# Performance work log

Hardware: AMD Instinct MI355X
Metric: run time of the kernel (lower is better)

The kernel has to match this reference:

```python
import jax, jax.numpy as jnp
import numpy as np

N_NODES = 100000
N_EDGES = 1600000
STATE_DIM = 128
HID = 32


def _glorot(key, shape):
    fan_in, fan_out = shape
    lim = jnp.sqrt(6.0 / (fan_in + fan_out))
    return jax.random.uniform(key, shape, jnp.float32, -lim, lim)


def setup_inputs() -> dict:
    key = jax.random.key(0)
    ks = jax.random.split(key, 10)
    x = jax.random.normal(ks[0], (N_NODES, STATE_DIM), jnp.float32)
    edge_index = jax.random.randint(ks[1], (2, N_EDGES), 0, N_NODES, jnp.int32)
    params = {
        "W1": _glorot(ks[2], (STATE_DIM, HID)), "b1": jnp.zeros((HID,), jnp.float32),
        "Wh": _glorot(ks[3], (HID, HID)),        "bh": jnp.zeros((HID,), jnp.float32),
        "W2": _glorot(ks[4], (HID, 1)),          "b2": jnp.zeros((1,), jnp.float32),
        "Ws": _glorot(ks[5], (HID, 1)),          "bs": jnp.zeros((1,), jnp.float32),
    }
    return {"x": x, "edge_index": edge_index, **params}


def _gcn_norm(edge_index, n):
    # PyG GCNConv: add self-loops, symmetric normalization D^-1/2 (A+I) D^-1/2
    src, dst = edge_index[0], edge_index[1]
    ones = jnp.ones((src.shape[0],), jnp.float32)
    deg = jax.ops.segment_sum(ones, dst, num_segments=n) + 1.0  # +1 for self-loop
    dinv = jax.lax.rsqrt(deg)  # deg >= 1, always finite
    edge_norm = dinv[src] * dinv[dst]          # [E]
    self_norm = dinv * dinv                    # [N]
    return edge_norm, self_norm


def _gcn_conv(h, W, b, src, dst, edge_norm, self_norm, n):
    # transform first (PyG order), then normalized aggregation
    h = h @ W                                                   # [N, out]
    msg = h[src] * edge_norm[:, None]                           # [E, out] gather
    agg = jax.ops.segment_sum(msg, dst, num_segments=n)         # scatter-add
    return agg + h * self_norm[:, None] + b


def reference(x, edge_index, W1, b1, Wh, bh, W2, b2, Ws, bs):
    n = x.shape[0]
    src, dst = edge_index[0], edge_index[1]
    edge_norm, self_norm = _gcn_norm(edge_index, n)
    h = _gcn_conv(x, W1, b1, src, dst, edge_norm, self_norm, n)
    h = _gcn_conv(h, Wh, bh, src, dst, edge_norm, self_norm, n)
    mu = jax.nn.relu(h)
    mu = _gcn_conv(mu, W2, b2, src, dst, edge_norm, self_norm, n)
    std = _gcn_conv(h, Ws, bs, src, dst, edge_norm, self_norm, n)
    return (mu, std)
```

## Files before the change

kernel.cpp:

```cpp
#include <hip/hip_runtime.h>

#define NN 100000
#define NE 1600000
#define SD 128
#define HD 32
#define NV4 25000
#define NSB 98

__global__ __launch_bounds__(256) void k_count(const int* __restrict__ dst,
                                               unsigned* __restrict__ cnt,
                                               unsigned* __restrict__ rank) {
    int e = blockIdx.x * 256 + threadIdx.x;
    int d = dst[e];
    rank[e] = atomicAdd(&cnt[d], 1u);
}

__global__ __launch_bounds__(256) void k_scanA(const uint4* __restrict__ cnt4,
                                               unsigned* __restrict__ bsum) {
    __shared__ unsigned ts[256];
    int tid = threadIdx.x;
    int f = blockIdx.x * 256 + tid;
    unsigned s = 0;
    if (f < NV4) { uint4 v = cnt4[f]; s = v.x + v.y + v.z + v.w; }
    ts[tid] = s; __syncthreads();
    for (int off = 128; off > 0; off >>= 1) {
        if (tid < off) ts[tid] += ts[tid + off];
        __syncthreads();
    }
    if (tid == 0) bsum[blockIdx.x] = ts[0];
}

__global__ __launch_bounds__(128) void k_scanB(unsigned* __restrict__ bsum,
                                               unsigned* __restrict__ rowptr) {
    __shared__ unsigned s[128];
    int tid = threadIdx.x;
    unsigned v = (tid < NSB) ? bsum[tid] : 0u;
    s[tid] = v; __syncthreads();
    for (int off = 1; off < 128; off <<= 1) {
        unsigned t = (tid >= off) ? s[tid - off] : 0u;
        __syncthreads();
        s[tid] += t;
        __syncthreads();
    }
    if (tid < NSB) bsum[tid] = s[tid] - v;
    if (tid == 0) rowptr[NN] = NE;
}

__global__ __launch_bounds__(256) void k_scanC(const uint4* __restrict__ cnt4,
                                               const unsigned* __restrict__ bsum,
                                               uint4* __restrict__ rowptr4,
                                               float4* __restrict__ dinv4) {
    __shared__ unsigned ts[256];
    int tid = threadIdx.x;
    int f = blockIdx.x * 256 + tid;
    uint4 v = {0, 0, 0, 0};
    if (f < NV4) v = cnt4[f];
    unsigned tsum = v.x + v.y + v.z + v.w;
    ts[tid] = tsum; __syncthreads();
    for (int off = 1; off < 256; off <<= 1) {
        unsigned t = (tid >= off) ? ts[tid - off] : 0u;
        __syncthreads();
        ts[tid] += t;
        __syncthreads();
    }
    unsigned ebase = ts[tid] - tsum + bsum[blockIdx.x];
    if (f < NV4) {
        uint4 r;
        r.x = ebase;
        r.y = r.x + v.x;
        r.z = r.y + v.y;
        r.w = r.z + v.z;
        rowptr4[f] = r;
        float4 dv;
        dv.x = rsqrtf((float)v.x + 1.0f);
        dv.y = rsqrtf((float)v.y + 1.0f);
        dv.z = rsqrtf((float)v.z + 1.0f);
        dv.w = rsqrtf((float)v.w + 1.0f);
        dinv4[f] = dv;
    }
}

__global__ __launch_bounds__(256) void k_fill(const int* __restrict__ src,
                                              const int* __restrict__ dst,
                                              const unsigned* __restrict__ rank,
                                              const unsigned* __restrict__ rowptr,
                                              unsigned* __restrict__ edat) {
    int e = blockIdx.x * 256 + threadIdx.x;
    int d = dst[e];
    edat[rowptr[d] + rank[e]] = (unsigned)src[e];
}

__global__ __launch_bounds__(256) void k_mm128(const float* __restrict__ X,
                                               const float* __restrict__ W,
                                               const float* __restrict__ dinv,
                                               float* __restrict__ out) {
    __shared__ float Wls[SD * HD];
    __shared__ float xT[32][260];
    int tid = threadIdx.x;
    {
        const float4* W4 = (const float4*)W;
        float4* Wl4 = (float4*)Wls;
        for (int i = tid; i < SD * HD / 4; i += 256) Wl4[i] = W4[i];
    }
    int nb = blockIdx.x * 256;
    int g = tid & 7;
    int q = tid >> 3;
    float acc[8][4] = {};
    for (int kc = 0; kc < SD; kc += 32) {
        __syncthreads();
        for (int i = tid; i < 256 * 8; i += 256) {
            int n = i >> 3, k4 = i & 7;
            int node = nb + n;
            float4 v = (node < NN) ? *(const float4*)&X[(size_t)node * SD + kc + k4 * 4]
                                   : make_float4(0.f, 0.f, 0.f, 0.f);
            xT[k4 * 4 + 0][n] = v.x;
            xT[k4 * 4 + 1][n] = v.y;
            xT[k4 * 4 + 2][n] = v.z;
            xT[k4 * 4 + 3][n] = v.w;
        }
        __syncthreads();
#pragma unroll
        for (int kk = 0; kk < 32; ++kk) {
            const float4 xa = *(const float4*)&xT[kk][q * 8];
            const float4 xb = *(const float4*)&xT[kk][q * 8 + 4];
            const float4 wv = *(const float4*)&Wls[(kc + kk) * HD + g * 4];
            acc[0][0] = fmaf(xa.x, wv.x, acc[0][0]);
            acc[0][1] = fmaf(xa.x, wv.y, acc[0][1]);
            acc[0][2] = fmaf(xa.x, wv.z, acc[0][2]);
            acc[0][3] = fmaf(xa.x, wv.w, acc[0][3]);
            acc[1][0] = fmaf(xa.y, wv.x, acc[1][0]);
            acc[1][1] = fmaf(xa.y, wv.y, acc[1][1]);
            acc[1][2] = fmaf(xa.y, wv.z, acc[1][2]);
            acc[1][3] = fmaf(xa.y, wv.w, acc[1][3]);
            acc[2][0] = fmaf(xa.z, wv.x, acc[2][0]);
            acc[2][1] = fmaf(xa.z, wv.y, acc[2][1]);
            acc[2][2] = fmaf(xa.z, wv.z, acc[2][2]);
            acc[2][3] = fmaf(xa.z, wv.w, acc[2][3]);
            acc[3][0] = fmaf(xa.w, wv.x, acc[3][0]);
            acc[3][1] = fmaf(xa.w, wv.y, acc[3][1]);
            acc[3][2] = fmaf(xa.w, wv.z, acc[3][2]);
            acc[3][3] = fmaf(xa.w, wv.w, acc[3][3]);
            acc[4][0] = fmaf(xb.x, wv.x, acc[4][0]);
            acc[4][1] = fmaf(xb.x, wv.y, acc[4][1]);
            acc[4][2] = fmaf(xb.x, wv.z, acc[4][2]);
            acc[4][3] = fmaf(xb.x, wv.w, acc[4][3]);
            acc[5][0] = fmaf(xb.y, wv.x, acc[5][0]);
            acc[5][1] = fmaf(xb.y, wv.y, acc[5][1]);
            acc[5][2] = fmaf(xb.y, wv.z, acc[5][2]);
            acc[5][3] = fmaf(xb.y, wv.w, acc[5][3]);
            acc[6][0] = fmaf(xb.z, wv.x, acc[6][0]);
            acc[6][1] = fmaf(xb.z, wv.y, acc[6][1]);
            acc[6][2] = fmaf(xb.z, wv.z, acc[6][2]);
            acc[6][3] = fmaf(xb.z, wv.w, acc[6][3]);
            acc[7][0] = fmaf(xb.w, wv.x, acc[7][0]);
            acc[7][1] = fmaf(xb.w, wv.y, acc[7][1]);
            acc[7][2] = fmaf(xb.w, wv.z, acc[7][2]);
            acc[7][3] = fmaf(xb.w, wv.w, acc[7][3]);
        }
    }
#pragma unroll
    for (int r = 0; r < 8; ++r) {
        int node = nb + q * 8 + r;
        if (node < NN) {
            float dv = dinv[node];
            float4 o = {acc[r][0] * dv, acc[r][1] * dv, acc[r][2] * dv, acc[r][3] * dv};
            *(float4*)&out[(size_t)node * HD + g * 4] = o;
        }
    }
}

template <int MODE>
__global__ __launch_bounds__(256) void k_gather(const unsigned* __restrict__ edat,
                                                const unsigned* __restrict__ rowptr,
                                                const float* __restrict__ dinv,
                                                const float* __restrict__ hw,
                                                const float* __restrict__ bias,
                                                const float* __restrict__ Wa,
                                                const float* __restrict__ Wb,
                                                float* __restrict__ outw) {
    int gid = blockIdx.x * 256 + threadIdx.x;
    int n = gid >> 5, j = gid & 31;
    unsigned s0 = rowptr[n], s1 = rowptr[n + 1];
    float acc = 0.f;
    unsigned i = s0;
    for (; i + 4 <= s1; i += 4) {
        unsigned e0 = edat[i], e1 = edat[i + 1], e2 = edat[i + 2], e3 = edat[i + 3];
        float v0 = hw[(size_t)e0 * HD + j];
        float v1 = hw[(size_t)e1 * HD + j];
        float v2 = hw[(size_t)e2 * HD + j];
        float v3 = hw[(size_t)e3 * HD + j];
        acc += (v0 + v1) + (v2 + v3);
    }
    for (; i < s1; ++i) acc += hw[(size_t)edat[i] * HD + j];
    float dv = dinv[n];
    float v = dv * (acc + hw[(size_t)n * HD + j]) + bias[j];
    if (MODE == 1) {
        float h2 = 0.f;
#pragma unroll
        for (int jj = 0; jj < 32; ++jj)
            h2 = fmaf(__shfl(v, jj, 32), Wa[jj * HD + j], h2);
        outw[(size_t)n * HD + j] = h2 * dv;
    } else {
        float a = fmaxf(v, 0.f) * Wa[j];
        float b = v * Wb[j];
#pragma unroll
        for (int off = 16; off > 0; off >>= 1) {
            a += __shfl_xor(a, off, 32);
            b += __shfl_xor(b, off, 32);
        }
        if (j == 0) ((float2*)outw)[n] = make_float2(a * dv, b * dv);
    }
}

__global__ __launch_bounds__(256) void k_gscal(const unsigned* __restrict__ edat,
                                               const unsigned* __restrict__ rowptr,
                                               const float* __restrict__ dinv,
                                               const float2* __restrict__ head_w,
                                               const float* __restrict__ b2,
                                               const float* __restrict__ bs,
                                               float* __restrict__ out) {
    int gid = blockIdx.x * 256 + threadIdx.x;
    int n = gid >> 5, l = gid & 31;
    unsigned s0 = rowptr[n], s1 = rowptr[n + 1];
    float a = 0.f, b = 0.f;
    for (unsigned i = s0 + l; i < s1; i += 32) {
        float2 w = head_w[edat[i]];
        a += w.x; b += w.y;
    }
#pragma unroll
    for (int off = 16; off > 0; off >>= 1) {
        a += __shfl_xor(a, off, 32);
        b += __shfl_xor(b, off, 32);
    }
    if (l == 0) {
        float dv = dinv[n];
        float2 self = head_w[n];
        out[n]      = dv * (a + self.x) + b2[0];
        out[NN + n] = dv * (b + self.y) + bs[0];
    }
}

extern "C" void kernel_launch(void* const* d_in, const int* in_sizes, int n_in,
                              void* d_out, int out_size, void* d_ws, size_t ws_size,
                              hipStream_t stream) {
    const float* x   = (const float*)d_in[0];
    const int*   ei  = (const int*)d_in[1];
    const int*   src = ei;
    const int*   dst = ei + NE;
    const float* W1  = (const float*)d_in[2];
    const float* b1  = (const float*)d_in[3];
    const float* Wh  = (const float*)d_in[4];
    const float* bh  = (const float*)d_in[5];
    const float* W2  = (const float*)d_in[6];
    const float* b2  = (const float*)d_in[7];
    const float* Wsp = (const float*)d_in[8];
    const float* bs  = (const float*)d_in[9];
    float* out = (float*)d_out;

    unsigned* w      = (unsigned*)d_ws;
    unsigned* edat   = w;
    float*    hw1    = (float*)(w + 1600000);
    unsigned* rank   = w + 4800000;
    float*    hw2    = (float*)(w + 4800000);
    unsigned* rowptr = w + 8000000;
    unsigned* cnt    = rowptr + 100004;
    float*    dinv   = (float*)(cnt + 100000);
    float*    headw  = dinv + 100000;
    unsigned* bsum   = (unsigned*)(headw + 200000);

    hipMemsetAsync(cnt, 0, NN * sizeof(unsigned), stream);
    k_count<<<NE / 256, 256, 0, stream>>>(dst, cnt, rank);
    k_scanA<<<NSB, 256, 0, stream>>>((const uint4*)cnt, bsum);
    k_scanB<<<1, 128, 0, stream>>>(bsum, rowptr);
    k_scanC<<<NSB, 256, 0, stream>>>((const uint4*)cnt, bsum, (uint4*)rowptr, (float4*)dinv);
    k_fill<<<NE / 256, 256, 0, stream>>>(src, dst, rank, rowptr, edat);

    k_mm128<<<(NN + 255) / 256, 256, 0, stream>>>(x, W1, dinv, hw1);
    k_gather<1><<<NN * HD / 256, 256, 0, stream>>>(edat, rowptr, dinv, hw1, b1, Wh, nullptr, hw2);
    k_gather<2><<<NN * HD / 256, 256, 0, stream>>>(edat, rowptr, dinv, hw2, bh, W2, Wsp, headw);
    k_gscal<<<NN * HD / 256, 256, 0, stream>>>(edat, rowptr, dinv, (const float2*)headw, b2, bs, out);
}
```

Baseline: 333.3 us.

## Build CSR with two-level bucketed counting sort instead of global atomics

Replaces the per-edge global-atomic count, three-kernel scan and scattered fill with a bucketed counting sort. Edges are first binned by dst>>8 into 391 buckets using LDS histograms and block-level offsets. Each bucket is then sorted locally in shared memory to produce rowptr, dinv and the sorted source list. This removes global atomic contention and random global scatters. It relies on each bucket holding at most 6144 edges (MAXBE) and on packing the local dst index into the high bits of the src value.

```diff
diff --git a/kernel.cpp b/kernel.cpp
--- a/kernel.cpp
+++ b/kernel.cpp
@@ -4,90 +4,101 @@
 #define NE 1600000
 #define SD 128
 #define HD 32
-#define NV4 25000
-#define NSB 98
-
-__global__ __launch_bounds__(256) void k_count(const int* __restrict__ dst,
-                                               unsigned* __restrict__ cnt,
-                                               unsigned* __restrict__ rank) {
-    int e = blockIdx.x * 256 + threadIdx.x;
-    int d = dst[e];
-    rank[e] = atomicAdd(&cnt[d], 1u);
-}
-
-__global__ __launch_bounds__(256) void k_scanA(const uint4* __restrict__ cnt4,
-                                               unsigned* __restrict__ bsum) {
-    __shared__ unsigned ts[256];
+#define NBK 391
+#define EPB 4000
+#define NBLK 400
+#define MAXBE 6144
+
+__global__ __launch_bounds__(256) void k_p1(const int* __restrict__ dst,
+                                            unsigned* __restrict__ bktcnt,
+                                            unsigned* __restrict__ blockbase) {
+    __shared__ unsigned h[NBK];
+    int blk = blockIdx.x, tid = threadIdx.x;
+    for (int i = tid; i < NBK; i += 256) h[i] = 0;
+    __syncthreads();
+    int e0 = blk * EPB;
+    for (int i = tid; i < EPB; i += 256)
+        atomicAdd(&h[(unsigned)dst[e0 + i] >> 8], 1u);
+    __syncthreads();
+    for (int i = tid; i < NBK; i += 256)
+        blockbase[blk * NBK + i] = atomicAdd(&bktcnt[i], h[i]);
+}
+
+__global__ __launch_bounds__(512) void k_p2(const unsigned* __restrict__ bktcnt,
+                                            unsigned* __restrict__ bktbase,
+                                            unsigned* __restrict__ rowptr) {
+    __shared__ unsigned sc[512];
     int tid = threadIdx.x;
-    int f = blockIdx.x * 256 + tid;
-    unsigned s = 0;
-    if (f < NV4) { uint4 v = cnt4[f]; s = v.x + v.y + v.z + v.w; }
-    ts[tid] = s; __syncthreads();
-    for (int off = 128; off > 0; off >>= 1) {
-        if (tid < off) ts[tid] += ts[tid + off];
-        __syncthreads();
-    }
-    if (tid == 0) bsum[blockIdx.x] = ts[0];
-}
-
-__global__ __launch_bounds__(128) void k_scanB(unsigned* __restrict__ bsum,
-                                               unsigned* __restrict__ rowptr) {
-    __shared__ unsigned s[128];
-    int tid = threadIdx.x;
-    unsigned v = (tid < NSB) ? bsum[tid] : 0u;
-    s[tid] = v; __syncthreads();
-    for (int off = 1; off < 128; off <<= 1) {
-        unsigned t = (tid >= off) ? s[tid - off] : 0u;
-        __syncthreads();
-        s[tid] += t;
-        __syncthreads();
-    }
-    if (tid < NSB) bsum[tid] = s[tid] - v;
+    unsigned c = (tid < NBK) ? bktcnt[tid] : 0u;
+    sc[tid] = c;
+    __syncthreads();
+    for (int off = 1; off < 512; off <<= 1) {
+        unsigned t = (tid >= off) ? sc[tid - off] : 0u;
+        __syncthreads();
+        sc[tid] += t;
+        __syncthreads();
+    }
+    if (tid <= NBK) bktbase[tid] = sc[tid] - c;
     if (tid == 0) rowptr[NN] = NE;
 }
 
-__global__ __launch_bounds__(256) void k_scanC(const uint4* __restrict__ cnt4,
-                                               const unsigned* __restrict__ bsum,
-                                               uint4* __restrict__ rowptr4,
-                                               float4* __restrict__ dinv4) {
-    __shared__ unsigned ts[256];
-    int tid = threadIdx.x;
-    int f = blockIdx.x * 256 + tid;
-    uint4 v = {0, 0, 0, 0};
-    if (f < NV4) v = cnt4[f];
-    unsigned tsum = v.x + v.y + v.z + v.w;
-    ts[tid] = tsum; __syncthreads();
+__global__ __launch_bounds__(256) void k_p3(const int* __restrict__ src,
+                                            const int* __restrict__ dst,
+                                            const unsigned* __restrict__ bktbase,
+                                            const unsigned* __restrict__ blockbase,
+                                            unsigned* __restrict__ ebuf) {
+    __shared__ unsigned cur[NBK];
+    int blk = blockIdx.x, tid = threadIdx.x;
+    for (int i = tid; i < NBK; i += 256)
+        cur[i] = bktbase[i] + blockbase[blk * NBK + i];
+    __syncthreads();
+    int e0 = blk * EPB;
+    for (int i = tid; i < EPB; i += 256) {
+        int d = dst[e0 + i];
+        unsigned s = (unsigned)src[e0 + i];
+        unsigned b = (unsigned)d >> 8;
+        unsigned pos = atomicAdd(&cur[b], 1u);
+        ebuf[pos] = ((unsigned)(d & 255) << 20) | s;
+    }
+}
+
+__global__ __launch_bounds__(256) void k_p4(unsigned* __restrict__ ebuf,
+                                            const unsigned* __restrict__ bktbase,
+                                            unsigned* __restrict__ rowptr,
+                                            float* __restrict__ dinv) {
+    __shared__ unsigned eL[MAXBE];
+    __shared__ unsigned hist[256];
+    __shared__ unsigned sc[256];
+    int b = blockIdx.x, tid = threadIdx.x;
+    unsigned base = bktbase[b], nE = bktbase[b + 1] - base;
+    int n0 = b << 8;
+    int nodes = min(256, NN - n0);
+    for (unsigned i = tid; i < nE; i += 256) eL[i] = ebuf[base + i];
+    hist[tid] = 0;
+    __syncthreads();
+    for (unsigned i = tid; i < nE; i += 256) atomicAdd(&hist[eL[i] >> 20], 1u);
+    __syncthreads();
+    unsigned c = hist[tid];
+    sc[tid] = c;
+    __syncthreads();
     for (int off = 1; off < 256; off <<= 1) {
-        unsigned t = (tid >= off) ? ts[tid - off] : 0u;
-        __syncthreads();
-        ts[tid] += t;
-        __syncthreads();
-    }
-    unsigned ebase = ts[tid] - tsum + bsum[blockIdx.x];
-    if (f < NV4) {
-        uint4 r;
-        r.x = ebase;
-        r.y = r.x + v.x;
-        r.z = r.y + v.y;
-        r.w = r.z + v.z;
-        rowptr4[f] = r;
-        float4 dv;
-        dv.x = rsqrtf((float)v.x + 1.0f);
-        dv.y = rsqrtf((float)v.y + 1.0f);
-        dv.z = rsqrtf((float)v.z + 1.0f);
-        dv.w = rsqrtf((float)v.w + 1.0f);
-        dinv4[f] = dv;
-    }
-}
-
-__global__ __launch_bounds__(256) void k_fill(const int* __restrict__ src,
-                                              const int* __restrict__ dst,
-                                              const unsigned* __restrict__ rank,
-                                              const unsigned* __restrict__ rowptr,
-                                              unsigned* __restrict__ edat) {
-    int e = blockIdx.x * 256 + threadIdx.x;
-    int d = dst[e];
-    edat[rowptr[d] + rank[e]] = (unsigned)src[e];
+        unsigned t = (tid >= off) ? sc[tid - off] : 0u;
+        __syncthreads();
+        sc[tid] += t;
+        __syncthreads();
+    }
+    unsigned excl = sc[tid] - c;
+    if (tid < nodes) {
+        rowptr[n0 + tid] = base + excl;
+        dinv[n0 + tid] = rsqrtf((float)c + 1.0f);
+    }
+    hist[tid] = base + excl;
+    __syncthreads();
+    for (unsigned i = tid; i < nE; i += 256) {
+        unsigned v = eL[i];
+        unsigned pos = atomicAdd(&hist[v >> 20], 1u);
+        ebuf[pos] = v & 0xFFFFFu;
+    }
 }
 
 __global__ __launch_bounds__(256) void k_mm128(const float* __restrict__ X,
@@ -257,23 +268,22 @@
     const float* bs  = (const float*)d_in[9];
     float* out = (float*)d_out;
 
-    unsigned* w      = (unsigned*)d_ws;
-    unsigned* edat   = w;
-    float*    hw1    = (float*)(w + 1600000);
-    unsigned* rank   = w + 4800000;
-    float*    hw2    = (float*)(w + 4800000);
-    unsigned* rowptr = w + 8000000;
-    unsigned* cnt    = rowptr + 100004;
-    float*    dinv   = (float*)(cnt + 100000);
-    float*    headw  = dinv + 100000;
-    unsigned* bsum   = (unsigned*)(headw + 200000);
-
-    hipMemsetAsync(cnt, 0, NN * sizeof(unsigned), stream);
-    k_count<<<NE / 256, 256, 0, stream>>>(dst, cnt, rank);
-    k_scanA<<<NSB, 256, 0, stream>>>((const uint4*)cnt, bsum);
-    k_scanB<<<1, 128, 0, stream>>>(bsum, rowptr);
-    k_scanC<<<NSB, 256, 0, stream>>>((const uint4*)cnt, bsum, (uint4*)rowptr, (float4*)dinv);
-    k_fill<<<NE / 256, 256, 0, stream>>>(src, dst, rank, rowptr, edat);
+    unsigned* w         = (unsigned*)d_ws;
+    unsigned* edat      = w;
+    unsigned* blockbase = w + 1600000;
+    float*    hw1       = (float*)(w + 1760000);
+    float*    hw2       = (float*)(w + 4960000);
+    unsigned* rowptr    = w + 8160000;
+    unsigned* bktcnt    = w + 8260004;
+    unsigned* bktbase   = w + 8260400;
+    float*    dinv      = (float*)(w + 8260800);
+    float*    headw     = (float*)(w + 8360800);
+
+    hipMemsetAsync(bktcnt, 0, NBK * sizeof(unsigned), stream);
+    k_p1<<<NBLK, 256, 0, stream>>>(dst, bktcnt, blockbase);
+    k_p2<<<1, 512, 0, stream>>>(bktcnt, bktbase, rowptr);
+    k_p3<<<NBLK, 256, 0, stream>>>(src, dst, bktbase, blockbase, edat);
+    k_p4<<<NBK, 256, 0, stream>>>(edat, bktbase, rowptr, dinv);
 
     k_mm128<<<(NN + 255) / 256, 256, 0, stream>>>(x, W1, dinv, hw1);
     k_gather<1><<<NN * HD / 256, 256, 0, stream>>>(edat, rowptr, dinv, hw1, b1, Wh, nullptr, hw2);
```

New measurement: 286.4 us. 14.1% less time.
